# Optimization experiments

Hardware: AMD Instinct MI355X
Metric: run time of the kernel (lower is better)

## Reference

```python
import jax, jax.numpy as jnp
import numpy as np
import math

B, N, L = 512, 50, 50
D = 128
N_ITEMS = 100000
N_INTENTS = 1024
MAX_LEN = 50
ALPHA = 0.5
STDV = 1.0 / math.sqrt(D)


def _uniform(key, shape):
    return jax.random.uniform(key, shape, dtype=jnp.float32, minval=-STDV, maxval=STDV)


def setup_inputs() -> dict:
    key = jax.random.key(0)
    ks = jax.random.split(key, 24)
    inp = {
        'items': jax.random.randint(ks[0], (B, N), 0, N_ITEMS, dtype=jnp.int64) if jax.config.jax_enable_x64 else jax.random.randint(ks[0], (B, N), 0, N_ITEMS).astype(jnp.int32),
        'A': jax.random.randint(ks[1], (B, N, N), 0, 3, dtype=jnp.int32),
        'inputs': jax.random.randint(ks[2], (B, L), 0, N_ITEMS).astype(jnp.int32),
        'masks': jnp.ones((B, L), dtype=jnp.int32),
        'alias_inputs': jax.random.randint(ks[3], (B, L), 0, N).astype(jnp.int32),
        'item_emb': _uniform(ks[4], (N_ITEMS, D)),
        'intent_emb': _uniform(ks[5], (N_INTENTS, D)),
        'pos_emb': _uniform(ks[6], (MAX_LEN + 1, D)),
        'lq': _uniform(ks[7], (D, D)),
        'lk': _uniform(ks[8], (D, D)),
        'la': _uniform(ks[9], (D,)),
        'lb': _uniform(ks[10], (D,)),
        'la1': _uniform(ks[11], (D,)),
        'la2': _uniform(ks[12], (D,)),
        'lb1': _uniform(ks[13], (D,)),
        'lb2': _uniform(ks[14], (D,)),
        'W1': _uniform(ks[15], (D, D)),
        'b1': _uniform(ks[16], (D,)),
        'W2': _uniform(ks[17], (D, D)),
        'b2': _uniform(ks[18], (D,)),
        'w3': _uniform(ks[19], (D,)),
    }
    inp['items'] = inp['items'].astype(jnp.int32)
    return inp


def _lrelu(x):
    return jnp.where(x >= 0, x, 0.2 * x)


def reference(items, A, inputs, masks, alias_inputs, item_emb, intent_emb, pos_emb,
              lq, lk, la, lb, la1, la2, lb1, lb2, W1, b1, W2, b2, w3):
    n_items, d = item_emb.shape
    n_intents = intent_emb.shape[0]
    # in-place weight L2 row-normalization from torch forward
    item_w = item_emb / jnp.linalg.norm(item_emb, axis=1, keepdims=True)
    intent_w = intent_emb / jnp.linalg.norm(intent_emb, axis=1, keepdims=True)

    # ---- IntentGraph: top-3 sparse routing (softmax is monotonic, topk on logits) ----
    sim = (item_w @ lq) @ (intent_w @ lk).T / jnp.sqrt(jnp.float32(d))  # [Ni, Nc]
    _, idx = jax.lax.top_k(sim, 3)  # [Ni, 3] intent ids per item
    item_idx = jnp.repeat(jnp.arange(n_items), 3)  # [E]
    intent_idx = idx.reshape(-1)                   # [E]

    # sparse softmax over items per intent row, then sparse mm -> new intent emb
    e1 = _lrelu((intent_w[intent_idx] * item_w[item_idx]) @ la)  # [E]
    m1 = jax.ops.segment_max(e1, intent_idx, num_segments=n_intents)
    ex1 = jnp.exp(e1 - m1[intent_idx])
    den1 = jax.ops.segment_sum(ex1, intent_idx, num_segments=n_intents)
    w1e = ex1 / den1[intent_idx]
    intent_new = jax.ops.segment_sum(w1e[:, None] * item_w[item_idx], intent_idx,
                                     num_segments=n_intents)  # [Nc, D]

    # sparse softmax over the 3 intents per item, sparse mm back to items
    nb = intent_new[idx]  # [Ni, 3, D]
    e2 = _lrelu((item_w[:, None, :] * nb) @ lb)  # [Ni, 3]
    w2 = jax.nn.softmax(e2, axis=1)
    item_nei = jnp.einsum('nk,nkd->nd', w2, nb)
    agg = ALPHA * item_w + (1.0 - ALPHA) * item_nei

    # ---- session-level ----
    h_intent = agg[items]   # [B, N, D]
    hi = item_w[items]      # [B, N, D]
    mf = masks.astype(item_w.dtype)  # [B, L]
    hs = (item_w[inputs] * mf[:, :, None]).sum(1) / mf.sum(1, keepdims=True)  # [B, D]

    # ---- LocalGraph: dense NxN attention, two edge types ----
    a1 = _lrelu(jnp.einsum('bid,bjd,d->bij', hi, hi, la1)
                + jnp.einsum('bd,bjd,d->bj', hs, hi, lb1)[:, None, :])
    a2 = _lrelu(jnp.einsum('bid,bjd,d->bij', hi, hi, la2)
                + jnp.einsum('bd,bjd,d->bj', hs, hi, lb2)[:, None, :])
    neg = jnp.float32(-9e15)
    att = jnp.where(A == 1, a1, neg)
    att = jnp.where(A == 2, a2, att)
    att = jax.nn.softmax(att, axis=2)
    h_local = att @ hi  # [B, N, D]

    output = h_local + h_intent + h_local * h_intent
    sessions = jnp.take_along_axis(output, alias_inputs[:, :, None], axis=1)  # [B, L, D]

    # ---- Readout ----
    Ls = alias_inputs.shape[1]
    spe = pos_emb[:Ls][None]  # [1, L, D]
    hir = sessions + spe
    hsr = (hir * mf[:, :, None]).sum(1) / mf.sum(1, keepdims=True)
    q1 = hir @ W1 + b1
    q2 = (hsr @ W2 + b2)[:, None, :]
    al = jax.nn.sigmoid(q1 + q2) @ w3  # [B, L]
    hf = (al[:, :, None] * sessions * mf[:, :, None]).sum(1)  # [B, D]
    pos_n = pos_emb[-1] * (spe * mf[:, :, None]).sum(1) / mf.sum(1, keepdims=True)
    hf = hf + pos_n
    scores = hf @ item_w[1:].T  # [B, n_items-1]
    return scores
```

## Files before the change

### kernel.cpp

```cpp
#include <hip/hip_runtime.h>
#include <math.h>

typedef __attribute__((ext_vector_type(4))) float f32x4;
typedef __attribute__((ext_vector_type(8))) short bf16x8;

static __device__ __forceinline__ unsigned short f2bf(float f) {
  unsigned int u = __float_as_uint(f);
  unsigned int r = (u + 0x7FFFu + ((u >> 16) & 1u)) >> 16;
  return (unsigned short)r;
}
static __device__ __forceinline__ float bf2f(unsigned short h) {
  return __uint_as_float(((unsigned int)h) << 16);
}

#define INS3(vv, cc) do { float _v=(vv); int _c=(cc); \
  if (_v > v2) { if (_v > v1) { v2=v1; c2=c1i; if (_v > v0) { v1=v0; c1i=c0; v0=_v; c0=_c; } \
  else { v1=_v; c1i=_c; } } else { v2=_v; c2=_c; } } } while(0)

#define INS4(vv, cc) do { float _v=(vv); int _c=(cc); \
  if (_v > w3v) { if (_v > w1v) { if (_v > w0v) { w3v=w2v;d3=d2; w2v=w1v;d2=d1; w1v=w0v;d1=d0; w0v=_v;d0=_c; } \
    else { w3v=w2v;d3=d2; w2v=w1v;d2=d1; w1v=_v;d1=_c; } } \
    else { if (_v > w2v) { w3v=w2v;d3=d2; w2v=_v;d2=_c; } else { w3v=_v; d3=_c; } } } } while(0)

__global__ __launch_bounds__(256) void k_norm(const float* __restrict__ in,
                                              float* __restrict__ out, int R) {
  int g = (blockIdx.x * 256 + threadIdx.x) >> 6;
  int lane = threadIdx.x & 63;
  if (g >= R) return;
  float2 v = ((const float2*)(in + (size_t)g * 128))[lane];
  float ss = v.x * v.x + v.y * v.y;
#pragma unroll
  for (int o = 32; o; o >>= 1) ss += __shfl_xor(ss, o, 64);
  float s = 1.0f / sqrtf(ss);
  ((float2*)(out + (size_t)g * 128))[lane] = make_float2(v.x * s, v.y * s);
}

__global__ __launch_bounds__(256) void k_prep_item(const float* __restrict__ in,
                                                   float* __restrict__ item_w,
                                                   unsigned short* __restrict__ itp, int R) {
  int g = (blockIdx.x * 256 + threadIdx.x) >> 6;
  int lane = threadIdx.x & 63;
  if (g >= R) return;
  float2 v = ((const float2*)(in + (size_t)g * 128))[lane];
  float ss = v.x * v.x + v.y * v.y;
#pragma unroll
  for (int o = 32; o; o >>= 1) ss += __shfl_xor(ss, o, 64);
  float s = 1.0f / sqrtf(ss);
  float x = v.x * s, y = v.y * s;
  ((float2*)(item_w + (size_t)g * 128))[lane] = make_float2(x, y);
  unsigned short hx = f2bf(x), hy = f2bf(y);
  unsigned short lx = f2bf(x - bf2f(hx)), ly = f2bf(y - bf2f(hy));
  unsigned short* row = itp + (size_t)g * 384;
  ((ushort2*)row)[lane] = make_ushort2(hx, hy);
  ((ushort2*)(row + 128))[lane] = make_ushort2(hx, hy);
  ((ushort2*)(row + 256))[lane] = make_ushort2(lx, ly);
}

__global__ __launch_bounds__(256) void k_split(const float* __restrict__ in,
                                               unsigned short* __restrict__ outp, int R) {
  int g = (blockIdx.x * 256 + threadIdx.x) >> 6;
  int lane = threadIdx.x & 63;
  if (g >= R) return;
  float2 v = ((const float2*)(in + (size_t)g * 128))[lane];
  unsigned short hx = f2bf(v.x), hy = f2bf(v.y);
  unsigned short lx = f2bf(v.x - bf2f(hx)), ly = f2bf(v.y - bf2f(hy));
  unsigned short* row = outp + (size_t)g * 384;
  ((ushort2*)row)[lane] = make_ushort2(hx, hy);
  ((ushort2*)(row + 128))[lane] = make_ushort2(lx, ly);
  ((ushort2*)(row + 256))[lane] = make_ushort2(hx, hy);
}

__global__ __launch_bounds__(256) void k_t128(const float* __restrict__ in,
                                              float* __restrict__ out) {
  for (int i = threadIdx.x; i < 128 * 128; i += 256) {
    int k = i >> 7, j = i & 127;
    out[j * 128 + k] = in[i];
  }
}

__global__ __launch_bounds__(256) void k_gemm_abt(const float* __restrict__ A,
                                                  const float* __restrict__ B,
                                                  float* __restrict__ C, int M, int N) {
  __shared__ float As[64][132];
  __shared__ float Bs[48][132];
  const int t = threadIdx.x;
  const int m0 = blockIdx.y * 64, n0 = blockIdx.x * 48;
  for (int i = t; i < 64 * 32; i += 256) {
    int r = i >> 5, c4 = (i & 31) << 2;
    float4 v = make_float4(0.f, 0.f, 0.f, 0.f);
    if (m0 + r < M) v = *(const float4*)(A + (size_t)(m0 + r) * 128 + c4);
    *(float4*)&As[r][c4] = v;
  }
  for (int i = t; i < 48 * 32; i += 256) {
    int r = i >> 5, c4 = (i & 31) << 2;
    float4 v = make_float4(0.f, 0.f, 0.f, 0.f);
    if (n0 + r < N) v = *(const float4*)(B + (size_t)(n0 + r) * 128 + c4);
    *(float4*)&Bs[r][c4] = v;
  }
  __syncthreads();
  const int ty = t >> 4, tx = t & 15;
  float acc[4][3];
#pragma unroll
  for (int i = 0; i < 4; i++)
#pragma unroll
    for (int j = 0; j < 3; j++) acc[i][j] = 0.f;
#pragma unroll 4
  for (int k = 0; k < 128; k += 4) {
    float4 a[4], b[3];
#pragma unroll
    for (int i = 0; i < 4; i++) a[i] = *(const float4*)&As[ty + 16 * i][k];
#pragma unroll
    for (int j = 0; j < 3; j++) b[j] = *(const float4*)&Bs[tx + 16 * j][k];
#pragma unroll
    for (int i = 0; i < 4; i++)
#pragma unroll
      for (int j = 0; j < 3; j++) {
        float s = acc[i][j];
        s = fmaf(a[i].x, b[j].x, s);
        s = fmaf(a[i].y, b[j].y, s);
        s = fmaf(a[i].z, b[j].z, s);
        s = fmaf(a[i].w, b[j].w, s);
        acc[i][j] = s;
      }
  }
#pragma unroll
  for (int i = 0; i < 4; i++) {
    int m = m0 + ty + 16 * i;
    if (m >= M) continue;
#pragma unroll
    for (int j = 0; j < 3; j++) {
      int n = n0 + tx + 16 * j;
      if (n < N) C[(size_t)m * N + n] = acc[i][j];
    }
  }
}

template <int MODE>
__global__ __launch_bounds__(256, 2) void k_mfma(const unsigned short* __restrict__ Abase,
                                                 const unsigned short* __restrict__ Bbase,
                                                 float* __restrict__ C, int ldc, int Nc,
                                                 int* __restrict__ pi4, int Mv) {
  __shared__ __align__(16) char lds[32768];
  const int t = threadIdx.x, l = t & 63, w = t >> 6;
  const int wr = w >> 1, wc = w & 1;

  int m0, n0, chunk = 0;
  {
    int g = blockIdx.x;
    int xcd = g & 7, r = g >> 3;
    if (MODE == 0) {
      chunk = r & 7;
      int mt = (r >> 3) * 8 + xcd;
      if (mt >= ((Mv + 127) >> 7)) return;
      m0 = mt << 7;
      n0 = chunk << 7;
    } else {
      int mq = r & 3;
      int nt = (r >> 2) * 8 + xcd;
      if (nt >= ((Nc + 127) >> 7)) return;
      m0 = mq << 7;
      n0 = nt << 7;
    }
  }
  const unsigned short* A = Abase + (size_t)m0 * 384;
  const unsigned short* B = Bbase + (size_t)n0 * 384;

  const int r1 = t >> 2, c1 = t & 3;
  f32x4 acc[4][4];
  {
    f32x4 z = {0.f, 0.f, 0.f, 0.f};
#pragma unroll
    for (int i = 0; i < 4; i++)
#pragma unroll
      for (int j = 0; j < 4; j++) acc[i][j] = z;
  }

  int4 sa0, sa1, sb0, sb1;
  {
    sa0 = *(const int4*)(A + (size_t)r1 * 384 + c1 * 8);
    sa1 = *(const int4*)(A + (size_t)(r1 + 64) * 384 + c1 * 8);
    sb0 = *(const int4*)(B + (size_t)r1 * 384 + c1 * 8);
    sb1 = *(const int4*)(B + (size_t)(r1 + 64) * 384 + c1 * 8);
  }

  for (int kt = 0; kt < 12; ++kt) {
    if (kt) __syncthreads();
    *(int4*)(lds + r1 * 80 + c1 * 16) = sa0;
    *(int4*)(lds + (r1 + 64) * 80 + c1 * 16) = sa1;
    *(int4*)(lds + 10240 + r1 * 80 + c1 * 16) = sb0;
    *(int4*)(lds + 10240 + (r1 + 64) * 80 + c1 * 16) = sb1;
    __syncthreads();
    if (kt < 11) {
      const unsigned short* ka = A + (kt + 1) * 32;
      const unsigned short* kb = B + (kt + 1) * 32;
      sa0 = *(const int4*)(ka + (size_t)r1 * 384 + c1 * 8);
      sa1 = *(const int4*)(ka + (size_t)(r1 + 64) * 384 + c1 * 8);
      sb0 = *(const int4*)(kb + (size_t)r1 * 384 + c1 * 8);
      sb1 = *(const int4*)(kb + (size_t)(r1 + 64) * 384 + c1 * 8);
    }
    bf16x8 af[4], bfr[4];
#pragma unroll
    for (int i = 0; i < 4; i++) {
      int ar = wr * 64 + i * 16 + (l & 15);
      af[i] = *(const bf16x8*)(lds + ar * 80 + (l >> 4) * 16);
      int br = wc * 64 + i * 16 + (l & 15);
      bfr[i] = *(const bf16x8*)(lds + 10240 + br * 80 + (l >> 4) * 16);
    }
#pragma unroll
    for (int i = 0; i < 4; i++)
#pragma unroll
      for (int j = 0; j < 4; j++)
        acc[i][j] = __builtin_amdgcn_mfma_f32_16x16x32_bf16(af[i], bfr[j], acc[i][j], 0, 0, 0);
  }

  if (MODE == 1) {
#pragma unroll
    for (int i = 0; i < 4; i++)
#pragma unroll
      for (int q = 0; q < 4; q++) {
        int m = m0 + wr * 64 + i * 16 + (l >> 4) * 4 + q;
#pragma unroll
        for (int j = 0; j < 4; j++) {
          int n = n0 + wc * 64 + j * 16 + (l & 15);
          if (n < Nc) C[(size_t)m * ldc + n] = acc[i][j][q];
        }
      }
  } else {
    __syncthreads();
    float* sp = (float*)lds;
#pragma unroll
    for (int i = 0; i < 4; i++)
#pragma unroll
      for (int q = 0; q < 4; q++) {
        float va = -3.0e38f, vb = -3.0e38f;
        int ja = 0, jb = 0;
#pragma unroll
        for (int j = 0; j < 4; j++) {
          float v = acc[i][j][q];
          if (v > vb) {
            if (v > va) { vb = va; jb = ja; va = v; ja = j; }
            else { vb = v; jb = j; }
          }
        }
        int row = wr * 64 + i * 16 + (l >> 4) * 4 + q;
        int contrib = wc * 16 + (l & 15);
        sp[(row * 32 + contrib) * 2] =
            __uint_as_float((__float_as_uint(va) & ~3u) | (unsigned)ja);
        sp[(row * 32 + contrib) * 2 + 1] =
            __uint_as_float((__float_as_uint(vb) & ~3u) | (unsigned)jb);
      }
    __syncthreads();
    if (t < 128) {
      int grow = m0 + t;
      if (grow < Mv) {
        float w0v = -3.0e38f, w1v = -3.0e38f, w2v = -3.0e38f, w3v = -3.0e38f;
        int d0 = 0, d1 = 0, d2 = 0, d3 = 0;
        for (int cbt = 0; cbt < 64; cbt++) {
          float v = sp[t * 64 + cbt];
          int contrib = cbt >> 1;
          int j = (int)(__float_as_uint(v) & 3u);
          int col = n0 + (contrib >> 4) * 64 + j * 16 + (contrib & 15);
          INS4(v, col);
        }
        size_t pb = (size_t)grow * 32 + chunk * 4;
        pi4[pb] = d0; pi4[pb + 1] = d1; pi4[pb + 2] = d2; pi4[pb + 3] = d3;
      }
    }
  }
}

__global__ __launch_bounds__(256) void k_rescore(const int* __restrict__ pi4,
                                                 const float* __restrict__ item_w,
                                                 const float* __restrict__ Gt,
                                                 const float* __restrict__ intw,
                                                 const float* __restrict__ la,
                                                 int* __restrict__ idx3,
                                                 float* __restrict__ e1vals,
                                                 int* __restrict__ cnt, int M) {
  int r = (blockIdx.x * 256 + threadIdx.x) >> 6;
  int l = threadIdx.x & 63;
  if (r >= M) return;
  float2 iw = ((const float2*)(item_w + (size_t)r * 128))[l];
  float v0 = -3.0e38f, v1 = -3.0e38f, v2 = -3.0e38f;
  int c0 = 0, c1i = 0, c2 = 0;
  for (int s = 0; s < 32; s++) {
    int c = pi4[(size_t)r * 32 + s];
    float2 g = ((const float2*)(Gt + (size_t)c * 128))[l];
    float d = iw.x * g.x + iw.y * g.y;
#pragma unroll
    for (int o = 32; o; o >>= 1) d += __shfl_xor(d, o, 64);
    INS3(d, c);
  }
  float2 lav = ((const float2*)la)[l];
  float e1v[3];
  int cs[3] = {c0, c1i, c2};
#pragma unroll
  for (int k = 0; k < 3; k++) {
    float2 cw = ((const float2*)(intw + (size_t)cs[k] * 128))[l];
    float d = iw.x * (cw.x * lav.x) + iw.y * (cw.y * lav.y);
#pragma unroll
    for (int o = 32; o; o >>= 1) d += __shfl_xor(d, o, 64);
    e1v[k] = d >= 0.f ? d : 0.2f * d;
  }
  if (l == 0) {
    idx3[r * 3] = c0; idx3[r * 3 + 1] = c1i; idx3[r * 3 + 2] = c2;
    e1vals[r * 3] = e1v[0]; e1vals[r * 3 + 1] = e1v[1]; e1vals[r * 3 + 2] = e1v[2];
    atomicAdd(&cnt[c0], 1); atomicAdd(&cnt[c1i], 1); atomicAdd(&cnt[c2], 1);
  }
}

__global__ __launch_bounds__(1024) void k_scan(const int* __restrict__ cnt,
                                               int* __restrict__ offs,
                                               int* __restrict__ cur) {
  __shared__ int s[1024];
  int t = threadIdx.x;
  int own = cnt[t];
  s[t] = own;
  __syncthreads();
  for (int o = 1; o < 1024; o <<= 1) {
    int v = (t >= o) ? s[t - o] : 0;
    __syncthreads();
    s[t] += v;
    __syncthreads();
  }
  int excl = s[t] - own;
  offs[t] = excl;
  cur[t] = excl;
  if (t == 1023) offs[1024] = s[1023];
}

__global__ void k_scatter(const int* __restrict__ idx3, int* __restrict__ cur,
                          int* __restrict__ edge_id, int E) {
  int e = blockIdx.x * 256 + threadIdx.x;
  if (e < E) {
    int c = idx3[e];
    int pos = atomicAdd(&cur[c], 1);
    edge_id[pos] = e;
  }
}

__global__ __launch_bounds__(512) void k_intent(const float* __restrict__ item_w,
                                                const float* __restrict__ e1vals,
                                                const int* __restrict__ offs,
                                                const int* __restrict__ edge_id,
                                                float* __restrict__ intent_new) {
  int c = blockIdx.x;
  int start = offs[c], end = offs[c + 1];
  int t = threadIdx.x, lane = t & 63, w = t >> 6;
  __shared__ float smx[8], sden[8], sacc[8][128];
  float mx = -3.0e38f;
  for (int e = start + t; e < end; e += 512) mx = fmaxf(mx, e1vals[edge_id[e]]);
#pragma unroll
  for (int o = 32; o; o >>= 1) mx = fmaxf(mx, __shfl_xor(mx, o, 64));
  if (lane == 0) smx[w] = mx;
  __syncthreads();
  mx = smx[0];
#pragma unroll
  for (int i = 1; i < 8; i++) mx = fmaxf(mx, smx[i]);
  float ax = 0.f, ay = 0.f, den = 0.f;
  int e = start + w;
  for (; e + 24 < end; e += 32) {
    int e0 = edge_id[e], e1 = edge_id[e + 8], e2 = edge_id[e + 16], e3 = edge_id[e + 24];
    float2 r0 = ((const float2*)(item_w + (size_t)((unsigned)e0 / 3u) * 128))[lane];
    float2 r1 = ((const float2*)(item_w + (size_t)((unsigned)e1 / 3u) * 128))[lane];
    float2 r2 = ((const float2*)(item_w + (size_t)((unsigned)e2 / 3u) * 128))[lane];
    float2 r3 = ((const float2*)(item_w + (size_t)((unsigned)e3 / 3u) * 128))[lane];
    float w0 = expf(e1vals[e0] - mx), w1 = expf(e1vals[e1] - mx);
    float w2 = expf(e1vals[e2] - mx), w3 = expf(e1vals[e3] - mx);
    ax = fmaf(w0, r0.x, fmaf(w1, r1.x, fmaf(w2, r2.x, fmaf(w3, r3.x, ax))));
    ay = fmaf(w0, r0.y, fmaf(w1, r1.y, fmaf(w2, r2.y, fmaf(w3, r3.y, ay))));
    den += w0 + w1 + w2 + w3;
  }
  for (; e < end; e += 8) {
    int e0 = edge_id[e];
    float2 r0 = ((const float2*)(item_w + (size_t)((unsigned)e0 / 3u) * 128))[lane];
    float w0 = expf(e1vals[e0] - mx);
    ax = fmaf(w0, r0.x, ax);
    ay = fmaf(w0, r0.y, ay);
    den += w0;
  }
  sacc[w][2 * lane] = ax;
  sacc[w][2 * lane + 1] = ay;
  if (lane == 0) sden[w] = den;
  __syncthreads();
  if (t < 128) {
    float s = 0.f;
#pragma unroll
    for (int i = 0; i < 8; i++) s += sacc[i][t];
    float dt = 0.f;
#pragma unroll
    for (int i = 0; i < 8; i++) dt += sden[i];
    float inv = dt > 0.f ? 1.f / dt : 0.f;
    intent_new[(size_t)c * 128 + t] = s * inv;
  }
}

__global__ __launch_bounds__(256) void k_hintent(const int* __restrict__ items,
                                                 const float* __restrict__ item_w,
                                                 const int* __restrict__ idx3,
                                                 const float* __restrict__ intent_new,
                                                 const float* __restrict__ lb,
                                                 float* __restrict__ h_intent, int total) {
  int g = (blockIdx.x * 256 + threadIdx.x) >> 6;
  int lane = threadIdx.x & 63;
  if (g >= total) return;
  int it = items[g];
  float2 iw = ((const float2*)(item_w + (size_t)it * 128))[lane];
  float2 lbv = ((const float2*)lb)[lane];
  float e2[3];
  float2 nb[3];
#pragma unroll
  for (int k = 0; k < 3; k++) {
    int c = idx3[(size_t)it * 3 + k];
    nb[k] = ((const float2*)(intent_new + (size_t)c * 128))[lane];
    float d = iw.x * nb[k].x * lbv.x + iw.y * nb[k].y * lbv.y;
#pragma unroll
    for (int o = 32; o; o >>= 1) d += __shfl_xor(d, o, 64);
    e2[k] = d >= 0.f ? d : 0.2f * d;
  }
  float m = fmaxf(fmaxf(e2[0], e2[1]), e2[2]);
  float x0 = expf(e2[0] - m), x1 = expf(e2[1] - m), x2 = expf(e2[2] - m);
  float inv = 1.f / (x0 + x1 + x2);
  float nx = (x0 * nb[0].x + x1 * nb[1].x + x2 * nb[2].x) * inv;
  float ny = (x0 * nb[0].y + x1 * nb[1].y + x2 * nb[2].y) * inv;
  ((float2*)(h_intent + (size_t)g * 128))[lane] =
      make_float2(0.5f * iw.x + 0.5f * nx, 0.5f * iw.y + 0.5f * ny);
}

__global__ __launch_bounds__(256) void k_session(
    const int* __restrict__ items, const int* __restrict__ Aadj,
    const int* __restrict__ inputs, const int* __restrict__ masks,
    const int* __restrict__ alias_inp, const float* __restrict__ item_w,
    const float* __restrict__ pos_emb, const float* __restrict__ la1,
    const float* __restrict__ la2, const float* __restrict__ lb1,
    const float* __restrict__ lb2, const float* __restrict__ W1,
    const float* __restrict__ b1, const float* __restrict__ W2,
    const float* __restrict__ b2, const float* __restrict__ w3,
    const float* __restrict__ h_intent, float* __restrict__ hf_out) {
  const int b = blockIdx.x;
  const int t = threadIdx.x;
  const int lane = t & 63, w = t >> 6;
  __shared__ float hi[50][128];
  __shared__ float outb[50][128];
  __shared__ float att[50][50];
  __shared__ float hsb[128], hsrb[128], q2b[128];
  __shared__ float cj1[50], cj2[50], alb[50];
  __shared__ float tmp2[2][128];
  __shared__ float wred[4][32];

  float mfs = 0.f;
  for (int l = 0; l < 50; l++) mfs += (float)masks[b * 50 + l];

  for (int i = t; i < 50 * 32; i += 256) {
    int r = i >> 5, c4 = (i & 31) << 2;
    int it = items[b * 50 + r];
    *(float4*)&hi[r][c4] = *(const float4*)(item_w + (size_t)it * 128 + c4);
  }
  {
    int d = t & 127, lh = t >> 7;
    float acc = 0.f;
    for (int l = lh; l < 50; l += 2) {
      float m = (float)masks[b * 50 + l];
      int row = inputs[b * 50 + l];
      acc += m * item_w[(size_t)row * 128 + d];
    }
    tmp2[lh][d] = acc;
  }
  __syncthreads();
  if (t < 128) hsb[t] = (tmp2[0][t] + tmp2[1][t]) / mfs;
  __syncthreads();
  {
    float2 lb1v = ((const float2*)lb1)[lane];
    float2 lb2v = ((const float2*)lb2)[lane];
    float2 hs2 = *(const float2*)&hsb[2 * lane];
    for (int j = w; j < 50; j += 4) {
      float2 xj = *(const float2*)&hi[j][2 * lane];
      float s1 = hs2.x * xj.x * lb1v.x + hs2.y * xj.y * lb1v.y;
      float s2 = hs2.x * xj.x * lb2v.x + hs2.y * xj.y * lb2v.y;
#pragma unroll
      for (int o = 32; o; o >>= 1) {
        s1 += __shfl_xor(s1, o, 64);
        s2 += __shfl_xor(s2, o, 64);
      }
      if (lane == 0) { cj1[j] = s1; cj2[j] = s2; }
    }
  }
  __syncthreads();
  {
    float2 la1v = ((const float2*)la1)[lane];
    float2 la2v = ((const float2*)la2)[lane];
    for (int i = w; i < 50; i += 4) {
      float2 xi = *(const float2*)&hi[i][2 * lane];
      float px1 = xi.x * la1v.x, py1 = xi.y * la1v.y;
      float px2 = xi.x * la2v.x, py2 = xi.y * la2v.y;
      for (int j = 0; j < 50; j++) {
        float2 xj = *(const float2*)&hi[j][2 * lane];
        float s1 = px1 * xj.x + py1 * xj.y;
        float s2 = px2 * xj.x + py2 * xj.y;
#pragma unroll
        for (int o = 32; o; o >>= 1) {
          s1 += __shfl_xor(s1, o, 64);
          s2 += __shfl_xor(s2, o, 64);
        }
        if (lane == 0) {
          int a = Aadj[((size_t)b * 50 + i) * 50 + j];
          float v;
          if (a == 1) { float x = s1 + cj1[j]; v = x >= 0.f ? x : 0.2f * x; }
          else if (a == 2) { float x = s2 + cj2[j]; v = x >= 0.f ? x : 0.2f * x; }
          else v = -9e15f;
          att[i][j] = v;
        }
      }
    }
  }
  __syncthreads();
  for (int i = w; i < 50; i += 4) {
    float v = lane < 50 ? att[i][lane] : -INFINITY;
    float mx = v;
#pragma unroll
    for (int o = 32; o; o >>= 1) mx = fmaxf(mx, __shfl_xor(mx, o, 64));
    float ex = lane < 50 ? expf(v - mx) : 0.f;
    float sm = ex;
#pragma unroll
    for (int o = 32; o; o >>= 1) sm += __shfl_xor(sm, o, 64);
    if (lane < 50) att[i][lane] = ex / sm;
  }
  __syncthreads();
  for (int i = w; i < 50; i += 4) {
    float ax = 0.f, ay = 0.f;
    for (int j = 0; j < 50; j++) {
      float a = att[i][j];
      float2 xj = *(const float2*)&hi[j][2 * lane];
      ax = fmaf(a, xj.x, ax);
      ay = fmaf(a, xj.y, ay);
    }
    float2 hv = ((const float2*)(h_intent + ((size_t)b * 50 + i) * 128))[lane];
    *(float2*)&outb[i][2 * lane] =
        make_float2(ax + hv.x + ax * hv.x, ay + hv.y + ay * hv.y);
  }
  __syncthreads();
  for (int i = t; i < 50 * 64; i += 256) {
    int r = i >> 6, c2 = (i & 63) << 1;
    int a = alias_inp[b * 50 + r];
    *(float2*)&hi[r][c2] = *(const float2*)&outb[a][c2];
  }
  __syncthreads();
  for (int i = t; i < 50 * 64; i += 256) {
    int r = i >> 6, c2 = (i & 63) << 1;
    float2 s = *(const float2*)&hi[r][c2];
    float2 p = *(const float2*)(pos_emb + (size_t)r * 128 + c2);
    *(float2*)&outb[r][c2] = make_float2(s.x + p.x, s.y + p.y);
  }
  __syncthreads();
  {
    int d = t & 127, lh = t >> 7;
    float acc = 0.f;
    for (int l = lh; l < 50; l += 2) acc += (float)masks[b * 50 + l] * outb[l][d];
    tmp2[lh][d] = acc;
  }
  __syncthreads();
  if (t < 128) hsrb[t] = (tmp2[0][t] + tmp2[1][t]) / mfs;
  __syncthreads();
  {
    int d = t & 127, kh = t >> 7;
    float acc = 0.f;
    for (int k = kh * 64; k < kh * 64 + 64; k++)
      acc = fmaf(hsrb[k], W2[(size_t)k * 128 + d], acc);
    tmp2[kh][d] = acc;
  }
  __syncthreads();
  if (t < 128) q2b[t] = b2[t] + tmp2[0][t] + tmp2[1][t];
  __syncthreads();
  {
    int d = t & 127, lh = t >> 7;
    float accq[25];
#pragma unroll
    for (int jj = 0; jj < 25; jj++) accq[jj] = b1[d];
    for (int k = 0; k < 128; k += 2) {
      float w1a = W1[(size_t)k * 128 + d];
      float w1b = W1[(size_t)(k + 1) * 128 + d];
#pragma unroll
      for (int jj = 0; jj < 25; jj++) {
        int l = lh + 2 * jj;
        float2 hv = *(const float2*)&outb[l][k];
        accq[jj] = fmaf(hv.x, w1a, accq[jj]);
        accq[jj] = fmaf(hv.y, w1b, accq[jj]);
      }
    }
    float w3v = w3[d], q2v = q2b[d];
#pragma unroll
    for (int jj = 0; jj < 25; jj++) {
      float s = 1.f / (1.f + expf(-(accq[jj] + q2v))) * w3v;
#pragma unroll
      for (int o = 32; o; o >>= 1) s += __shfl_xor(s, o, 64);
      if (lane == 0) wred[w][jj] = s;
    }
  }
  __syncthreads();
  if (t < 50) {
    int l = t, jj = l >> 1;
    alb[l] = (l & 1) ? (wred[2][jj] + wred[3][jj]) : (wred[0][jj] + wred[1][jj]);
  }
  __syncthreads();
  if (t < 128) {
    int d = t;
    float acc = 0.f, pacc = 0.f;
    for (int l = 0; l < 50; l++) {
      float m = (float)masks[b * 50 + l];
      acc += alb[l] * hi[l][d] * m;
      pacc += pos_emb[(size_t)l * 128 + d] * m;
    }
    hf_out[(size_t)b * 128 + d] = acc + pos_emb[50 * 128 + d] * (pacc / mfs);
  }
}

extern "C" void kernel_launch(void* const* d_in, const int* in_sizes, int n_in,
                              void* d_out, int out_size, void* d_ws, size_t ws_size,
                              hipStream_t stream) {
  const int* items = (const int*)d_in[0];
  const int* Aadj = (const int*)d_in[1];
  const int* inputs = (const int*)d_in[2];
  const int* masks = (const int*)d_in[3];
  const int* alias = (const int*)d_in[4];
  const float* item_emb = (const float*)d_in[5];
  const float* intent_emb = (const float*)d_in[6];
  const float* pos_emb = (const float*)d_in[7];
  const float* lq = (const float*)d_in[8];
  const float* lk = (const float*)d_in[9];
  const float* la = (const float*)d_in[10];
  const float* lb = (const float*)d_in[11];
  const float* la1 = (const float*)d_in[12];
  const float* la2 = (const float*)d_in[13];
  const float* lb1 = (const float*)d_in[14];
  const float* lb2 = (const float*)d_in[15];
  const float* W1 = (const float*)d_in[16];
  const float* b1 = (const float*)d_in[17];
  const float* W2 = (const float*)d_in[18];
  const float* b2 = (const float*)d_in[19];
  const float* w3 = (const float*)d_in[20];
  float* out = (float*)d_out;

  char* p = (char*)d_ws;
  auto alloc = [&](size_t bytes) {
    char* r = p;
    p += (bytes + 511) & ~(size_t)511;
    return r;
  };
  float* item_w = (float*)alloc(100000ull * 128 * 4);
  unsigned short* itp = (unsigned short*)alloc(100104ull * 384 * 2);
  unsigned short* gtp = (unsigned short*)alloc(1024ull * 384 * 2);
  float* intw = (float*)alloc(1024ull * 128 * 4);
  float* CK = (float*)alloc(1024ull * 128 * 4);
  float* Gt = (float*)alloc(1024ull * 128 * 4);
  float* lkT = (float*)alloc(128 * 128 * 4);
  int* idx3 = (int*)alloc(300000ull * 4);
  float* e1vals = (float*)alloc(300000ull * 4);
  int* cnt = (int*)alloc(1024 * 4);
  int* offs = (int*)alloc(1025 * 4);
  int* cur = (int*)alloc(1024 * 4);
  int* edge_id = (int*)alloc(300000ull * 4);
  char* big = alloc(13107200);
  int* pi4 = (int*)big;
  float* h_int = (float*)big;
  float* hf = (float*)alloc(512 * 128 * 4);
  float* hfp_f = (float*)alloc(512ull * 384 * 2);
  unsigned short* hfp = (unsigned short*)hfp_f;

  k_prep_item<<<25000, 256, 0, stream>>>(item_emb, item_w, itp, 100000);
  k_norm<<<256, 256, 0, stream>>>(intent_emb, intw, 1024);
  k_t128<<<1, 256, 0, stream>>>(lk, lkT);
  k_gemm_abt<<<dim3(3, 16), 256, 0, stream>>>(intw, lkT, CK, 1024, 128);
  k_gemm_abt<<<dim3(3, 16), 256, 0, stream>>>(CK, lq, Gt, 1024, 128);
  k_split<<<256, 256, 0, stream>>>(Gt, gtp, 1024);

  hipMemsetAsync(cnt, 0, 1024 * 4, stream);
  k_mfma<0><<<6272, 256, 0, stream>>>(itp, gtp, nullptr, 0, 1024, pi4, 100000);
  k_rescore<<<25000, 256, 0, stream>>>(pi4, item_w, Gt, intw, la, idx3, e1vals, cnt, 100000);

  k_scan<<<1, 1024, 0, stream>>>(cnt, offs, cur);
  k_scatter<<<(300000 + 255) / 256, 256, 0, stream>>>(idx3, cur, edge_id, 300000);
  k_intent<<<1024, 512, 0, stream>>>(item_w, e1vals, offs, edge_id, (float*)CK);
  k_hintent<<<6400, 256, 0, stream>>>(items, item_w, idx3, (float*)CK, lb, h_int, 25600);
  k_session<<<512, 256, 0, stream>>>(items, Aadj, inputs, masks, alias, item_w, pos_emb,
                                     la1, la2, lb1, lb2, W1, b1, W2, b2, w3, h_int, hf);
  k_split<<<128, 256, 0, stream>>>(hf, hfp, 512);
  k_mfma<1><<<3136, 256, 0, stream>>>(hfp, itp + 384, out, 99999, 99999, nullptr, 512);
}
```

Before: 1.351 ms.

## Restructure session attention with transposed hi layout and a 512-thread block

The per-session kernel now builds a transposed copy of the node embeddings in shared memory. Each lane computes one attention logit column by a serial dot product over D, which removes the per-pair wave shuffle reductions. Logit computation is fused with the masked softmax, dropping one pass and one barrier. The block grows to 512 threads, with the reductions and the W1 readout loop re-split across 8 waves. Shared buffers are aliased to keep the LDS footprint in check, and the serial 128-step loops with strided LDS reads may cause bank conflicts.

Measured after the change: 1.133 ms. 16.1% less time.

```diff
diff --git a/kernel.cpp b/kernel.cpp
--- a/kernel.cpp
+++ b/kernel.cpp
@@ -427,7 +427,7 @@
       make_float2(0.5f * iw.x + 0.5f * nx, 0.5f * iw.y + 0.5f * ny);
 }
 
-__global__ __launch_bounds__(256) void k_session(
+__global__ __launch_bounds__(512) void k_session(
     const int* __restrict__ items, const int* __restrict__ Aadj,
     const int* __restrict__ inputs, const int* __restrict__ masks,
     const int* __restrict__ alias_inp, const float* __restrict__ item_w,
@@ -441,81 +441,74 @@
   const int t = threadIdx.x;
   const int lane = t & 63, w = t >> 6;
   __shared__ float hi[50][128];
-  __shared__ float outb[50][128];
-  __shared__ float att[50][50];
+  __shared__ float outb[6400];
+  __shared__ float attb[2504];
   __shared__ float hsb[128], hsrb[128], q2b[128];
-  __shared__ float cj1[50], cj2[50], alb[50];
-  __shared__ float tmp2[2][128];
-  __shared__ float wred[4][32];
+  __shared__ float cj1v[50], cj2v[50], alb[50];
+  __shared__ float4 lab[128];
+
+  float* hiT = outb;
+  float* att = attb;
+  float* tmp4 = attb;
+  float* wred = attb + 512;
 
   float mfs = 0.f;
   for (int l = 0; l < 50; l++) mfs += (float)masks[b * 50 + l];
 
-  for (int i = t; i < 50 * 32; i += 256) {
+  for (int i = t; i < 50 * 32; i += 512) {
     int r = i >> 5, c4 = (i & 31) << 2;
     int it = items[b * 50 + r];
     *(float4*)&hi[r][c4] = *(const float4*)(item_w + (size_t)it * 128 + c4);
   }
+  if (t < 128) lab[t] = make_float4(la1[t], la2[t], lb1[t], lb2[t]);
   {
-    int d = t & 127, lh = t >> 7;
+    int d = t & 127, g = t >> 7;
     float acc = 0.f;
-    for (int l = lh; l < 50; l += 2) {
+    for (int l = g; l < 50; l += 4) {
       float m = (float)masks[b * 50 + l];
       int row = inputs[b * 50 + l];
       acc += m * item_w[(size_t)row * 128 + d];
     }
-    tmp2[lh][d] = acc;
-  }
-  __syncthreads();
-  if (t < 128) hsb[t] = (tmp2[0][t] + tmp2[1][t]) / mfs;
-  __syncthreads();
-  {
-    float2 lb1v = ((const float2*)lb1)[lane];
-    float2 lb2v = ((const float2*)lb2)[lane];
-    float2 hs2 = *(const float2*)&hsb[2 * lane];
-    for (int j = w; j < 50; j += 4) {
-      float2 xj = *(const float2*)&hi[j][2 * lane];
-      float s1 = hs2.x * xj.x * lb1v.x + hs2.y * xj.y * lb1v.y;
-      float s2 = hs2.x * xj.x * lb2v.x + hs2.y * xj.y * lb2v.y;
-#pragma unroll
-      for (int o = 32; o; o >>= 1) {
-        s1 += __shfl_xor(s1, o, 64);
-        s2 += __shfl_xor(s2, o, 64);
-      }
-      if (lane == 0) { cj1[j] = s1; cj2[j] = s2; }
-    }
-  }
-  __syncthreads();
-  {
-    float2 la1v = ((const float2*)la1)[lane];
-    float2 la2v = ((const float2*)la2)[lane];
-    for (int i = w; i < 50; i += 4) {
-      float2 xi = *(const float2*)&hi[i][2 * lane];
-      float px1 = xi.x * la1v.x, py1 = xi.y * la1v.y;
-      float px2 = xi.x * la2v.x, py2 = xi.y * la2v.y;
-      for (int j = 0; j < 50; j++) {
-        float2 xj = *(const float2*)&hi[j][2 * lane];
-        float s1 = px1 * xj.x + py1 * xj.y;
-        float s2 = px2 * xj.x + py2 * xj.y;
-#pragma unroll
-        for (int o = 32; o; o >>= 1) {
-          s1 += __shfl_xor(s1, o, 64);
-          s2 += __shfl_xor(s2, o, 64);
-        }
-        if (lane == 0) {
-          int a = Aadj[((size_t)b * 50 + i) * 50 + j];
-          float v;
-          if (a == 1) { float x = s1 + cj1[j]; v = x >= 0.f ? x : 0.2f * x; }
-          else if (a == 2) { float x = s2 + cj2[j]; v = x >= 0.f ? x : 0.2f * x; }
-          else v = -9e15f;
-          att[i][j] = v;
-        }
-      }
-    }
-  }
-  __syncthreads();
-  for (int i = w; i < 50; i += 4) {
-    float v = lane < 50 ? att[i][lane] : -INFINITY;
+    tmp4[g * 128 + d] = acc;
+  }
+  __syncthreads();
+  if (t < 128) hsb[t] = (tmp4[t] + tmp4[128 + t] + tmp4[256 + t] + tmp4[384 + t]) / mfs;
+  for (int i = t; i < 6400; i += 512) {
+    int r = i >> 7, d = i & 127;
+    hiT[d * 50 + r] = hi[r][d];
+  }
+  __syncthreads();
+  if (w == 0) {
+    int jc = lane < 50 ? lane : 49;
+    float s1 = 0.f, s2 = 0.f;
+#pragma unroll 8
+    for (int d = 0; d < 128; d++) {
+      float xj = hiT[d * 50 + jc];
+      float4 c = lab[d];
+      float hv = hsb[d];
+      s1 = fmaf(hv * c.z, xj, s1);
+      s2 = fmaf(hv * c.w, xj, s2);
+    }
+    if (lane < 50) { cj1v[lane] = s1; cj2v[lane] = s2; }
+  }
+  __syncthreads();
+  for (int i = w; i < 50; i += 8) {
+    int jc = lane < 50 ? lane : 49;
+    float s1 = 0.f, s2 = 0.f;
+#pragma unroll 8
+    for (int d = 0; d < 128; d++) {
+      float xi = hiT[d * 50 + i];
+      float4 c = lab[d];
+      float xj = hiT[d * 50 + jc];
+      s1 = fmaf(xi * c.x, xj, s1);
+      s2 = fmaf(xi * c.y, xj, s2);
+    }
+    float v = -9e15f;
+    if (lane < 50) {
+      int a = Aadj[((size_t)b * 50 + i) * 50 + lane];
+      if (a == 1) { float x = s1 + cj1v[lane]; v = x >= 0.f ? x : 0.2f * x; }
+      else if (a == 2) { float x = s2 + cj2v[lane]; v = x >= 0.f ? x : 0.2f * x; }
+    }
     float mx = v;
 #pragma unroll
     for (int o = 32; o; o >>= 1) mx = fmaxf(mx, __shfl_xor(mx, o, 64));
@@ -523,83 +516,84 @@
     float sm = ex;
 #pragma unroll
     for (int o = 32; o; o >>= 1) sm += __shfl_xor(sm, o, 64);
-    if (lane < 50) att[i][lane] = ex / sm;
-  }
-  __syncthreads();
-  for (int i = w; i < 50; i += 4) {
+    if (lane < 50) att[i * 50 + lane] = ex / sm;
+  }
+  __syncthreads();
+  for (int i = w; i < 50; i += 8) {
     float ax = 0.f, ay = 0.f;
     for (int j = 0; j < 50; j++) {
-      float a = att[i][j];
+      float a = att[i * 50 + j];
       float2 xj = *(const float2*)&hi[j][2 * lane];
       ax = fmaf(a, xj.x, ax);
       ay = fmaf(a, xj.y, ay);
     }
     float2 hv = ((const float2*)(h_intent + ((size_t)b * 50 + i) * 128))[lane];
-    *(float2*)&outb[i][2 * lane] =
+    *(float2*)&outb[i * 128 + 2 * lane] =
         make_float2(ax + hv.x + ax * hv.x, ay + hv.y + ay * hv.y);
   }
   __syncthreads();
-  for (int i = t; i < 50 * 64; i += 256) {
+  for (int i = t; i < 50 * 64; i += 512) {
     int r = i >> 6, c2 = (i & 63) << 1;
     int a = alias_inp[b * 50 + r];
-    *(float2*)&hi[r][c2] = *(const float2*)&outb[a][c2];
-  }
-  __syncthreads();
-  for (int i = t; i < 50 * 64; i += 256) {
+    *(float2*)&hi[r][c2] = *(const float2*)&outb[a * 128 + c2];
+  }
+  __syncthreads();
+  for (int i = t; i < 50 * 64; i += 512) {
     int r = i >> 6, c2 = (i & 63) << 1;
     float2 s = *(const float2*)&hi[r][c2];
-    float2 p = *(const float2*)(pos_emb + (size_t)r * 128 + c2);
-    *(float2*)&outb[r][c2] = make_float2(s.x + p.x, s.y + p.y);
+    float2 pp = *(const float2*)(pos_emb + (size_t)r * 128 + c2);
+    *(float2*)&outb[r * 128 + c2] = make_float2(s.x + pp.x, s.y + pp.y);
   }
   __syncthreads();
   {
-    int d = t & 127, lh = t >> 7;
+    int d = t & 127, g = t >> 7;
     float acc = 0.f;
-    for (int l = lh; l < 50; l += 2) acc += (float)masks[b * 50 + l] * outb[l][d];
-    tmp2[lh][d] = acc;
-  }
-  __syncthreads();
-  if (t < 128) hsrb[t] = (tmp2[0][t] + tmp2[1][t]) / mfs;
+    for (int l = g; l < 50; l += 4) acc += (float)masks[b * 50 + l] * outb[l * 128 + d];
+    tmp4[g * 128 + d] = acc;
+  }
+  __syncthreads();
+  if (t < 128) hsrb[t] = (tmp4[t] + tmp4[128 + t] + tmp4[256 + t] + tmp4[384 + t]) / mfs;
   __syncthreads();
   {
-    int d = t & 127, kh = t >> 7;
+    int d = t & 127, g = t >> 7;
     float acc = 0.f;
-    for (int k = kh * 64; k < kh * 64 + 64; k++)
+    for (int k = g * 32; k < g * 32 + 32; k++)
       acc = fmaf(hsrb[k], W2[(size_t)k * 128 + d], acc);
-    tmp2[kh][d] = acc;
-  }
-  __syncthreads();
-  if (t < 128) q2b[t] = b2[t] + tmp2[0][t] + tmp2[1][t];
+    tmp4[g * 128 + d] = acc;
+  }
+  __syncthreads();
+  if (t < 128) q2b[t] = b2[t] + tmp4[t] + tmp4[128 + t] + tmp4[256 + t] + tmp4[384 + t];
   __syncthreads();
   {
-    int d = t & 127, lh = t >> 7;
-    float accq[25];
-#pragma unroll
-    for (int jj = 0; jj < 25; jj++) accq[jj] = b1[d];
+    int d = t & 127, g = t >> 7;
+    float accq[13];
+#pragma unroll
+    for (int jj = 0; jj < 13; jj++) accq[jj] = b1[d];
     for (int k = 0; k < 128; k += 2) {
       float w1a = W1[(size_t)k * 128 + d];
       float w1b = W1[(size_t)(k + 1) * 128 + d];
 #pragma unroll
-      for (int jj = 0; jj < 25; jj++) {
-        int l = lh + 2 * jj;
-        float2 hv = *(const float2*)&outb[l][k];
+      for (int jj = 0; jj < 13; jj++) {
+        int l = g + 4 * jj;
+        int le = l < 50 ? l : 0;
+        float2 hv = *(const float2*)&outb[le * 128 + k];
         accq[jj] = fmaf(hv.x, w1a, accq[jj]);
         accq[jj] = fmaf(hv.y, w1b, accq[jj]);
       }
     }
     float w3v = w3[d], q2v = q2b[d];
 #pragma unroll
-    for (int jj = 0; jj < 25; jj++) {
+    for (int jj = 0; jj < 13; jj++) {
       float s = 1.f / (1.f + expf(-(accq[jj] + q2v))) * w3v;
 #pragma unroll
       for (int o = 32; o; o >>= 1) s += __shfl_xor(s, o, 64);
-      if (lane == 0) wred[w][jj] = s;
+      if (lane == 0) wred[w * 13 + jj] = s;
     }
   }
   __syncthreads();
   if (t < 50) {
-    int l = t, jj = l >> 1;
-    alb[l] = (l & 1) ? (wred[2][jj] + wred[3][jj]) : (wred[0][jj] + wred[1][jj]);
+    int g = t & 3, jj = t >> 2;
+    alb[t] = wred[(2 * g) * 13 + jj] + wred[(2 * g + 1) * 13 + jj];
   }
   __syncthreads();
   if (t < 128) {
@@ -681,7 +675,7 @@
   k_scatter<<<(300000 + 255) / 256, 256, 0, stream>>>(idx3, cur, edge_id, 300000);
   k_intent<<<1024, 512, 0, stream>>>(item_w, e1vals, offs, edge_id, (float*)CK);
   k_hintent<<<6400, 256, 0, stream>>>(items, item_w, idx3, (float*)CK, lb, h_int, 25600);
-  k_session<<<512, 256, 0, stream>>>(items, Aadj, inputs, masks, alias, item_w, pos_emb,
+  k_session<<<512, 512, 0, stream>>>(items, Aadj, inputs, masks, alias, item_w, pos_emb,
                                      la1, la2, lb1, lb2, W1, b1, W2, b2, w3, h_int, hf);
   k_split<<<128, 256, 0, stream>>>(hf, hfp, 512);
   k_mfma<1><<<3136, 256, 0, stream>>>(hfp, itp + 384, out, 99999, 99999, nullptr, 512);
```
